# Kernel tuning notes

Measured on AMD Instinct MI355X. Metric: run time of the kernel, lower is better.

The kernel has to match this reference:

```python
import jax, jax.numpy as jnp
import numpy as np

N = 100_000      # nodes (single heterogeneous node type)
E = 1_600_000    # edges per relation (avg in-degree ~16)
D = 128          # in_feats
H = 128          # rep_dim
R = 3            # relations


def setup_inputs() -> dict:
    key = jax.random.key(0)
    ks = jax.random.split(key, 1 + 6 * R)
    inp = {"x": jax.random.normal(ks[0], (N, D), jnp.float32)}
    for r in range(R):
        k = ks[1 + 6 * r: 1 + 6 * (r + 1)]
        inp[f"src{r}"] = jax.random.randint(k[0], (E,), 0, N)
        inp[f"dst{r}"] = jax.random.randint(k[1], (E,), 0, N)
        inp[f"w{r}"] = jax.random.uniform(k[2], (E,), jnp.float32)
        inp[f"Wself{r}"] = jax.random.normal(k[3], (D, H), jnp.float32) * 0.05
        inp[f"Wneigh{r}"] = jax.random.normal(k[4], (D, H), jnp.float32) * 0.05
        inp[f"b{r}"] = jax.random.normal(k[5], (H,), jnp.float32) * 0.05
    return inp


def _sage_mean(x, src, dst, w, Wself, Wneigh, b):
    """DGL SAGEConv, aggregator='mean', edge_weight=w, activation=ReLU.

    h_N[v] = (sum_{e:(u->v)} w_e * x[u]) / max(in_deg(v), 1)
    out    = relu(x @ Wself + h_N @ Wneigh + b)
    """
    msg = x[src] * w[:, None]                                   # [E, D] gather
    s = jax.ops.segment_sum(msg, dst, num_segments=N)           # [N, D] scatter-add
    deg = jax.ops.segment_sum(jnp.ones_like(w), dst, num_segments=N)  # [N]
    h_neigh = s / jnp.maximum(deg, 1.0)[:, None]                # mean; 0 for isolated nodes
    return jax.nn.relu(x @ Wself + h_neigh @ Wneigh + b)


def reference(x,
              src0, dst0, w0,
              src1, dst1, w1,
              src2, dst2, w2,
              Wself0, Wneigh0, b0,
              Wself1, Wneigh1, b1,
              Wself2, Wneigh2, b2):
    # HeteroGraphConv(aggregate='mean'): average the per-relation SAGEConv outputs.
    o0 = _sage_mean(x, src0, dst0, w0, Wself0, Wneigh0, b0)
    o1 = _sage_mean(x, src1, dst1, w1, Wself1, Wneigh1, b1)
    o2 = _sage_mean(x, src2, dst2, w2, Wself2, Wneigh2, b2)
    return (o0 + o1 + o2) / 3.0
```

## Files before the change

### kernel.cpp

```cpp
#include <hip/hip_runtime.h>
#include <hip/hip_bf16.h>
#include <cstdio>
#include <cstdint>
#include <cstddef>

#define NN 100000
#define EE 1600000
#define DD 128

#define BKT 196
#define RSHIFT 9
#define RANGE 512
#define CAP 9500
#define EPB 2048
#define ABLK ((EE + EPB - 1) / EPB)

typedef __attribute__((ext_vector_type(8))) short short8;
typedef __attribute__((ext_vector_type(4))) float floatx4;

__device__ __forceinline__ float bf2f(unsigned short u) {
    union { unsigned int u; float f; } c;
    c.u = ((unsigned int)u) << 16;
    return c.f;
}
__device__ __forceinline__ unsigned short f2bf(float f) {
    union { float f; unsigned int u; } c;
    c.f = f;
    unsigned int lsb = (c.u >> 16) & 1u;
    c.u += 0x7fffu + lsb;
    return (unsigned short)(c.u >> 16);
}

__global__ void detect_kernel(const void* x, const void* w, const void* Wm,
                              const void* b, int* flags) {
    __shared__ int ok_s;
    int bid = blockIdx.x, tid = threadIdx.x;
    if (tid == 0) ok_s = 0;
    __syncthreads();
    const unsigned short* p;
    int n;
    if (bid == 0)      { p = (const unsigned short*)x;  n = 1024; }
    else if (bid == 1) { p = (const unsigned short*)w;  n = 1024; }
    else if (bid == 2) { p = (const unsigned short*)Wm; n = 1024; }
    else               { p = (const unsigned short*)b;  n = 128;  }
    int ok = 0;
    for (int i = tid; i < n; i += blockDim.x) {
        unsigned short u = p[i];
        int e = (u >> 7) & 0xff;
        if (u == 0 || u == 0x8000 || (e >= 90 && e <= 127)) ok++;
    }
    atomicAdd(&ok_s, ok);
    __syncthreads();
    if (tid == 0) flags[bid] = (ok_s * 4 >= n * 3) ? 1 : 0;
}

__global__ void conv_x_kernel(const void* src, unsigned short* dst, int n4,
                              const int* flag) {
    if (*flag) return;
    int i = blockIdx.x * blockDim.x + threadIdx.x;
    if (i >= n4) return;
    float4 f = ((const float4*)src)[i];
    uint2 o;
    o.x = (unsigned int)f2bf(f.x) | ((unsigned int)f2bf(f.y) << 16);
    o.y = (unsigned int)f2bf(f.z) | ((unsigned int)f2bf(f.w) << 16);
    ((uint2*)dst)[i] = o;
}

__global__ void conv_f32_kernel(const void* src, float* dst, int n,
                                const int* flag) {
    int i = blockIdx.x * blockDim.x + threadIdx.x;
    if (i >= n) return;
    if (*flag) dst[i] = bf2f(((const unsigned short*)src)[i]);
    else       dst[i] = ((const float*)src)[i];
}

__global__ void conv_transposeW_kernel(const void* W, unsigned short* wT,
                                       const int* flag) {
    int i = blockIdx.x * blockDim.x + threadIdx.x;
    int d = i >> 7, h = i & 127;
    unsigned short v;
    if (*flag) v = ((const unsigned short*)W)[i];
    else       v = f2bf(((const float*)W)[i]);
    wT[h * DD + d] = v;
}

__global__ void __launch_bounds__(256) binscatter_kernel(
    const int* __restrict__ srcp, const int* __restrict__ dstp,
    const void* __restrict__ wp, int* __restrict__ gcur,
    int2* __restrict__ ebin, const int* __restrict__ wflag) {
    __shared__ int hist[BKT];
    __shared__ int off[BKT];
    __shared__ int cur[BKT];
    __shared__ int gbase[BKT];
    __shared__ int scan[256];
    __shared__ int2 sorted[EPB];
    __shared__ unsigned char slotb[EPB];
    const int tid = threadIdx.x;
    const int base = blockIdx.x * EPB;
    for (int i = tid; i < BKT; i += 256) hist[i] = 0;
    __syncthreads();
    int myd[8];
#pragma unroll
    for (int k = 0; k < 8; k++) {
        int i = base + k * 256 + tid;
        int d = (i < EE) ? dstp[i] : -1;
        myd[k] = d;
        if (d >= 0) atomicAdd(&hist[d >> RSHIFT], 1);
    }
    __syncthreads();
    int hv = (tid < BKT) ? hist[tid] : 0;
    scan[tid] = hv;
    __syncthreads();
    for (int o = 1; o < 256; o <<= 1) {
        int v = (tid >= o) ? scan[tid - o] : 0;
        __syncthreads();
        scan[tid] += v;
        __syncthreads();
    }
    if (tid < BKT) { off[tid] = scan[tid] - hv; cur[tid] = scan[tid] - hv; }
    __syncthreads();
    const bool wbf = (*wflag != 0);
#pragma unroll
    for (int k = 0; k < 8; k++) {
        int d = myd[k];
        if (d < 0) continue;
        int i = base + k * 256 + tid;
        int b = d >> RSHIFT;
        int dloc = d - (b << RSHIFT);
        int s = srcp[i];
        float wv = wbf ? bf2f(((const unsigned short*)wp)[i])
                       : ((const float*)wp)[i];
        union { float f; int i; } c; c.f = wv;
        int pos = atomicAdd(&cur[b], 1);
        sorted[pos] = make_int2(s | (dloc << 17), c.i);
        slotb[pos] = (unsigned char)b;
    }
    __syncthreads();
    if (tid < BKT) {
        int cnt = hist[tid];
        gbase[tid] = cnt ? atomicAdd(&gcur[tid], cnt) : 0;
    }
    __syncthreads();
    const int total = min(EPB, EE - base);
    for (int i = tid; i < total; i += 256) {
        int b = slotb[i];
        int g = gbase[b] + (i - off[b]);
        if (g < CAP) ebin[(size_t)b * CAP + g] = sorted[i];
    }
}

__global__ void __launch_bounds__(256) bucketsort_kernel(
    const int2* __restrict__ ebin, const int* __restrict__ gcur,
    int2* __restrict__ es2, int2* __restrict__ ptrv) {
    __shared__ int hc[RANGE];
    __shared__ int off[RANGE];
    __shared__ int scan[256];
    const int b = blockIdx.x, tid = threadIdx.x;
    const int base = b * CAP;
    const int cnt = min(gcur[b], CAP);
    for (int i = tid; i < RANGE; i += 256) hc[i] = 0;
    __syncthreads();
    for (int i = tid; i < cnt; i += 256) {
        int dl = ebin[base + i].x >> 17;
        atomicAdd(&hc[dl], 1);
    }
    __syncthreads();
    int a0 = hc[2 * tid], a1 = hc[2 * tid + 1];
    scan[tid] = a0 + a1;
    __syncthreads();
    for (int o = 1; o < 256; o <<= 1) {
        int v = (tid >= o) ? scan[tid - o] : 0;
        __syncthreads();
        scan[tid] += v;
        __syncthreads();
    }
    int ex = scan[tid] - (a0 + a1);
    off[2 * tid] = ex;
    off[2 * tid + 1] = ex + a0;
    ptrv[b * RANGE + 2 * tid]     = make_int2(base + ex, a0);
    ptrv[b * RANGE + 2 * tid + 1] = make_int2(base + ex + a0, a1);
    __syncthreads();
    hc[2 * tid] = off[2 * tid];
    hc[2 * tid + 1] = off[2 * tid + 1];
    __syncthreads();
    for (int i = tid; i < cnt; i += 256) {
        int2 rec = ebin[base + i];
        int dl = rec.x >> 17;
        int p = atomicAdd(&hc[dl], 1);
        es2[base + p] = make_int2(rec.x & 0x1FFFF, rec.y);
    }
}

__global__ void __launch_bounds__(256) aggregate_kernel(
    const int2* __restrict__ es, const int2* __restrict__ ptrv,
    const unsigned short* __restrict__ xc, const void* __restrict__ xraw,
    const int* __restrict__ xflag, unsigned short* __restrict__ hout) {
    int wave = (blockIdx.x * blockDim.x + threadIdx.x) >> 6;
    int lane = threadIdx.x & 63;
    if (wave >= NN) return;
    const unsigned int* x32 = (*xflag) ? (const unsigned int*)xraw
                                       : (const unsigned int*)xc;
    int2 pc = ptrv[wave];
    int beg = pc.x, deg = pc.y, end = beg + deg;
    float a0 = 0.f, a1 = 0.f;
    int e = beg;
    for (; e + 4 <= end; e += 4) {
        int2 e0 = es[e], e1 = es[e + 1], e2 = es[e + 2], e3 = es[e + 3];
        unsigned int p0 = x32[(size_t)e0.x * 64 + lane];
        unsigned int p1 = x32[(size_t)e1.x * 64 + lane];
        unsigned int p2 = x32[(size_t)e2.x * 64 + lane];
        unsigned int p3 = x32[(size_t)e3.x * 64 + lane];
        union { int i; float f; } c0, c1, c2, c3;
        c0.i = e0.y; c1.i = e1.y; c2.i = e2.y; c3.i = e3.y;
        a0 += c0.f * bf2f((unsigned short)(p0 & 0xffff));
        a1 += c0.f * bf2f((unsigned short)(p0 >> 16));
        a0 += c1.f * bf2f((unsigned short)(p1 & 0xffff));
        a1 += c1.f * bf2f((unsigned short)(p1 >> 16));
        a0 += c2.f * bf2f((unsigned short)(p2 & 0xffff));
        a1 += c2.f * bf2f((unsigned short)(p2 >> 16));
        a0 += c3.f * bf2f((unsigned short)(p3 & 0xffff));
        a1 += c3.f * bf2f((unsigned short)(p3 >> 16));
    }
    for (; e < end; e++) {
        int2 e0 = es[e];
        unsigned int p0 = x32[(size_t)e0.x * 64 + lane];
        union { int i; float f; } c0; c0.i = e0.y;
        a0 += c0.f * bf2f((unsigned short)(p0 & 0xffff));
        a1 += c0.f * bf2f((unsigned short)(p0 >> 16));
    }
    float inv = 1.0f / (float)(deg > 1 ? deg : 1);
    unsigned int outv = ((unsigned int)f2bf(a1 * inv) << 16) | f2bf(a0 * inv);
    ((unsigned int*)hout)[(size_t)wave * 64 + lane] = outv;
}

__global__ void __launch_bounds__(256) output_kernel(
    const unsigned short* __restrict__ xc, const void* __restrict__ xraw,
    const unsigned short* __restrict__ h, const unsigned short* __restrict__ wT,
    const float* __restrict__ bc, void* out, const int* __restrict__ flag) {
    __shared__ unsigned short lds[DD * 136];
    const int tid = threadIdx.x;
    const int wv = tid >> 6, lane = tid & 63;
    const int tile = blockIdx.x * 4 + wv;
    const bool active = tile < (NN / 16);
    const int c = lane & 15, q = lane >> 4;
    const int nodeRow = tile * 16 + c;
    const int xbf = *flag;
    const unsigned short* xs = xbf ? (const unsigned short*)xraw : xc;

    short8 xfrag[4];
    if (active) {
#pragma unroll
        for (int kc = 0; kc < 4; kc++)
            xfrag[kc] = *(const short8*)(xs + (size_t)nodeRow * DD + kc * 32 +
                                         q * 8);
    }

    floatx4 outacc[8];
#pragma unroll
    for (int i = 0; i < 8; i++) outacc[i] = (floatx4){0.f, 0.f, 0.f, 0.f};

    for (int r = 0; r < 3; r++) {
        floatx4 acc[8];
#pragma unroll
        for (int i = 0; i < 8; i++) acc[i] = (floatx4){0.f, 0.f, 0.f, 0.f};
        for (int p = 0; p < 2; p++) {
            const unsigned short* Wg = wT + (size_t)(r * 2 + p) * DD * DD;
            __syncthreads();
            for (int chunk = tid; chunk < DD * DD / 8; chunk += 256) {
                int row = chunk >> 4, col8 = chunk & 15;
                short8 v = *(const short8*)(Wg + row * DD + col8 * 8);
                *(short8*)(&lds[row * 136 + col8 * 8]) = v;
            }
            __syncthreads();
            if (active) {
#pragma unroll
                for (int kc = 0; kc < 4; kc++) {
                    short8 afrag;
                    if (p == 0) {
                        afrag = xfrag[kc];
                    } else {
                        afrag = *(const short8*)(h + (size_t)r * NN * DD +
                                                 (size_t)nodeRow * DD +
                                                 kc * 32 + q * 8);
                    }
#pragma unroll
                    for (int nt = 0; nt < 8; nt++) {
                        short8 bfrag = *(const short8*)(
                            &lds[(nt * 16 + c) * 136 + kc * 32 + q * 8]);
                        acc[nt] = __builtin_amdgcn_mfma_f32_16x16x32_bf16(
                            afrag, bfrag, acc[nt], 0, 0, 0);
                    }
                }
            }
        }
        if (active) {
#pragma unroll
            for (int nt = 0; nt < 8; nt++) {
                float bv = bc[r * DD + nt * 16 + c];
#pragma unroll
                for (int i = 0; i < 4; i++) {
                    float v = acc[nt][i] + bv;
                    outacc[nt][i] += fmaxf(v, 0.f);
                }
            }
        }
    }
    if (active) {
        const float sc = 1.f / 3.f;
        if (xbf) {
            unsigned short* o = (unsigned short*)out;
#pragma unroll
            for (int nt = 0; nt < 8; nt++)
#pragma unroll
                for (int i = 0; i < 4; i++)
                    o[(size_t)(tile * 16 + q * 4 + i) * DD + nt * 16 + c] =
                        f2bf(outacc[nt][i] * sc);
        } else {
            float* o = (float*)out;
#pragma unroll
            for (int nt = 0; nt < 8; nt++)
#pragma unroll
                for (int i = 0; i < 4; i++)
                    o[(size_t)(tile * 16 + q * 4 + i) * DD + nt * 16 + c] =
                        outacc[nt][i] * sc;
        }
    }
}

extern "C" void kernel_launch(void* const* d_in, const int* in_sizes, int n_in,
                              void* d_out, int out_size, void* d_ws,
                              size_t ws_size, hipStream_t stream) {
    char* w = (char*)d_ws;
    size_t off = 0;
    auto alloc = [&](size_t bytes) {
        size_t o = off;
        off = (off + bytes + 255) & ~(size_t)255;
        return o;
    };
    size_t o_flags = alloc(4 * sizeof(int));
    size_t o_gcur  = alloc(BKT * sizeof(int));
    size_t o_bc    = alloc(3 * DD * sizeof(float));
    size_t o_wT    = alloc(6 * DD * DD * sizeof(unsigned short));
    size_t o_xc    = alloc((size_t)NN * DD * sizeof(unsigned short));
    size_t o_ebin  = alloc((size_t)BKT * CAP * sizeof(int2));
    size_t o_es2   = alloc((size_t)BKT * CAP * sizeof(int2));
    size_t o_ptrv  = alloc((size_t)BKT * RANGE * sizeof(int2));
    size_t o_h     = alloc((size_t)3 * NN * DD * sizeof(unsigned short));
    if (ws_size < off) {
        fprintf(stderr, "kernel_launch: ws_size=%zu < needed=%zu\n", ws_size,
                off);
        return;
    }
    int* flags          = (int*)(w + o_flags);
    int* gcur           = (int*)(w + o_gcur);
    float* bc           = (float*)(w + o_bc);
    unsigned short* wT  = (unsigned short*)(w + o_wT);
    unsigned short* xc  = (unsigned short*)(w + o_xc);
    int2* ebin          = (int2*)(w + o_ebin);
    int2* es2           = (int2*)(w + o_es2);
    int2* ptrv          = (int2*)(w + o_ptrv);
    unsigned short* hh  = (unsigned short*)(w + o_h);

    const void* x_in = d_in[0];

    detect_kernel<<<4, 256, 0, stream>>>(x_in, d_in[3], d_in[4], d_in[6],
                                         flags);
    conv_x_kernel<<<(NN * DD / 4 + 255) / 256, 256, 0, stream>>>(
        x_in, xc, NN * DD / 4, flags + 0);
    for (int r = 0; r < 3; r++) {
        int base = 1 + 6 * r;
        conv_transposeW_kernel<<<64, 256, 0, stream>>>(
            d_in[base + 3], wT + (size_t)(r * 2 + 0) * DD * DD, flags + 2);
        conv_transposeW_kernel<<<64, 256, 0, stream>>>(
            d_in[base + 4], wT + (size_t)(r * 2 + 1) * DD * DD, flags + 2);
        conv_f32_kernel<<<1, 128, 0, stream>>>(d_in[base + 5], bc + r * DD, DD,
                                               flags + 3);
    }

    for (int r = 0; r < 3; r++) {
        int base = 1 + 6 * r;
        const int* srcp = (const int*)d_in[base + 0];
        const int* dstp = (const int*)d_in[base + 1];
        hipMemsetAsync(gcur, 0, BKT * sizeof(int), stream);
        binscatter_kernel<<<ABLK, 256, 0, stream>>>(srcp, dstp, d_in[base + 2],
                                                    gcur, ebin, flags + 1);
        bucketsort_kernel<<<BKT, 256, 0, stream>>>(ebin, gcur, es2, ptrv);
        aggregate_kernel<<<(NN + 3) / 4, 256, 0, stream>>>(
            es2, ptrv, xc, x_in, flags + 0, hh + (size_t)r * NN * DD);
    }

    const int NTILES = NN / 16;
    output_kernel<<<(NTILES + 3) / 4, 256, 0, stream>>>(
        xc, x_in, hh, wT, bc, d_out, flags + 0);
}
```

Measured before the change: 616.7 us.

## Replace atomic bucket offsets with count-scan-place pass; unroll gather loop by 8

Splits the edge bucketing into three kernels: a per-block histogram, a per-bucket scan across blocks, and a placement pass that reads precomputed bases. This removes the global atomicAdd and the memset, and makes bucket order deterministic, but reads dst twice and adds two kernel launches per relation. The aggregation loop is unrolled from 4 to 8 edges to keep more gathers in flight, and the bf16 unpack is done with simpler bit ops.

```diff
diff --git a/kernel.cpp b/kernel.cpp
--- a/kernel.cpp
+++ b/kernel.cpp
@@ -21,6 +21,16 @@
 __device__ __forceinline__ float bf2f(unsigned short u) {
     union { unsigned int u; float f; } c;
     c.u = ((unsigned int)u) << 16;
+    return c.f;
+}
+__device__ __forceinline__ float hi2f(unsigned int p) {
+    union { unsigned int u; float f; } c;
+    c.u = p & 0xffff0000u;
+    return c.f;
+}
+__device__ __forceinline__ float lo2f(unsigned int p) {
+    union { unsigned int u; float f; } c;
+    c.u = p << 16;
     return c.f;
 }
 __device__ __forceinline__ unsigned short f2bf(float f) {
@@ -84,9 +94,58 @@
     wT[h * DD + d] = v;
 }
 
-__global__ void __launch_bounds__(256) binscatter_kernel(
+__global__ void __launch_bounds__(256) countA_kernel(
+    const int* __restrict__ dstp, int* __restrict__ cnts) {
+    __shared__ int hist[BKT];
+    const int tid = threadIdx.x;
+    const int base = blockIdx.x * EPB;
+    for (int i = tid; i < BKT; i += 256) hist[i] = 0;
+    __syncthreads();
+#pragma unroll
+    for (int k = 0; k < 8; k++) {
+        int i = base + k * 256 + tid;
+        if (i < EE) atomicAdd(&hist[dstp[i] >> RSHIFT], 1);
+    }
+    __syncthreads();
+    for (int i = tid; i < BKT; i += 256)
+        cnts[(size_t)blockIdx.x * BKT + i] = hist[i];
+}
+
+__global__ void __launch_bounds__(256) scanA_kernel(
+    const int* __restrict__ cnts, int* __restrict__ bases,
+    int* __restrict__ gcur) {
+    __shared__ int s[256];
+    const int b = blockIdx.x, tid = threadIdx.x;
+    const int per = (ABLK + 255) / 256;
+    int v[4];
+    int sum = 0;
+#pragma unroll
+    for (int k = 0; k < 4; k++) {
+        int idx = tid * per + k;
+        v[k] = (idx < ABLK) ? cnts[(size_t)idx * BKT + b] : 0;
+        sum += v[k];
+    }
+    s[tid] = sum;
+    __syncthreads();
+    for (int o = 1; o < 256; o <<= 1) {
+        int t = (tid >= o) ? s[tid - o] : 0;
+        __syncthreads();
+        s[tid] += t;
+        __syncthreads();
+    }
+    int running = s[tid] - sum;
+#pragma unroll
+    for (int k = 0; k < 4; k++) {
+        int idx = tid * per + k;
+        if (idx < ABLK) bases[(size_t)idx * BKT + b] = running;
+        running += v[k];
+    }
+    if (tid == 255) gcur[b] = s[255];
+}
+
+__global__ void __launch_bounds__(256) placeA_kernel(
     const int* __restrict__ srcp, const int* __restrict__ dstp,
-    const void* __restrict__ wp, int* __restrict__ gcur,
+    const void* __restrict__ wp, const int* __restrict__ bases,
     int2* __restrict__ ebin, const int* __restrict__ wflag) {
     __shared__ int hist[BKT];
     __shared__ int off[BKT];
@@ -117,7 +176,11 @@
         scan[tid] += v;
         __syncthreads();
     }
-    if (tid < BKT) { off[tid] = scan[tid] - hv; cur[tid] = scan[tid] - hv; }
+    if (tid < BKT) {
+        off[tid] = scan[tid] - hv;
+        cur[tid] = scan[tid] - hv;
+        gbase[tid] = bases[(size_t)blockIdx.x * BKT + tid];
+    }
     __syncthreads();
     const bool wbf = (*wflag != 0);
 #pragma unroll
@@ -136,11 +199,6 @@
         slotb[pos] = (unsigned char)b;
     }
     __syncthreads();
-    if (tid < BKT) {
-        int cnt = hist[tid];
-        gbase[tid] = cnt ? atomicAdd(&gcur[tid], cnt) : 0;
-    }
-    __syncthreads();
     const int total = min(EPB, EE - base);
     for (int i = tid; i < total; i += 256) {
         int b = slotb[i];
@@ -204,29 +262,43 @@
     int beg = pc.x, deg = pc.y, end = beg + deg;
     float a0 = 0.f, a1 = 0.f;
     int e = beg;
-    for (; e + 4 <= end; e += 4) {
-        int2 e0 = es[e], e1 = es[e + 1], e2 = es[e + 2], e3 = es[e + 3];
-        unsigned int p0 = x32[(size_t)e0.x * 64 + lane];
-        unsigned int p1 = x32[(size_t)e1.x * 64 + lane];
-        unsigned int p2 = x32[(size_t)e2.x * 64 + lane];
-        unsigned int p3 = x32[(size_t)e3.x * 64 + lane];
-        union { int i; float f; } c0, c1, c2, c3;
-        c0.i = e0.y; c1.i = e1.y; c2.i = e2.y; c3.i = e3.y;
-        a0 += c0.f * bf2f((unsigned short)(p0 & 0xffff));
-        a1 += c0.f * bf2f((unsigned short)(p0 >> 16));
-        a0 += c1.f * bf2f((unsigned short)(p1 & 0xffff));
-        a1 += c1.f * bf2f((unsigned short)(p1 >> 16));
-        a0 += c2.f * bf2f((unsigned short)(p2 & 0xffff));
-        a1 += c2.f * bf2f((unsigned short)(p2 >> 16));
-        a0 += c3.f * bf2f((unsigned short)(p3 & 0xffff));
-        a1 += c3.f * bf2f((unsigned short)(p3 >> 16));
-    }
-    for (; e < end; e++) {
-        int2 e0 = es[e];
-        unsigned int p0 = x32[(size_t)e0.x * 64 + lane];
-        union { int i; float f; } c0; c0.i = e0.y;
-        a0 += c0.f * bf2f((unsigned short)(p0 & 0xffff));
-        a1 += c0.f * bf2f((unsigned short)(p0 >> 16));
+    for (; e + 8 <= end; e += 8) {
+        int2 r0 = es[e],     r1 = es[e + 1], r2 = es[e + 2], r3 = es[e + 3];
+        int2 r4 = es[e + 4], r5 = es[e + 5], r6 = es[e + 6], r7 = es[e + 7];
+        unsigned int p0 = x32[(size_t)r0.x * 64 + lane];
+        unsigned int p1 = x32[(size_t)r1.x * 64 + lane];
+        unsigned int p2 = x32[(size_t)r2.x * 64 + lane];
+        unsigned int p3 = x32[(size_t)r3.x * 64 + lane];
+        unsigned int p4 = x32[(size_t)r4.x * 64 + lane];
+        unsigned int p5 = x32[(size_t)r5.x * 64 + lane];
+        unsigned int p6 = x32[(size_t)r6.x * 64 + lane];
+        unsigned int p7 = x32[(size_t)r7.x * 64 + lane];
+        union { int i; float f; } c0, c1, c2, c3, c4, c5, c6, c7;
+        c0.i = r0.y; c1.i = r1.y; c2.i = r2.y; c3.i = r3.y;
+        c4.i = r4.y; c5.i = r5.y; c6.i = r6.y; c7.i = r7.y;
+        a0 += c0.f * lo2f(p0); a1 += c0.f * hi2f(p0);
+        a0 += c1.f * lo2f(p1); a1 += c1.f * hi2f(p1);
+        a0 += c2.f * lo2f(p2); a1 += c2.f * hi2f(p2);
+        a0 += c3.f * lo2f(p3); a1 += c3.f * hi2f(p3);
+        a0 += c4.f * lo2f(p4); a1 += c4.f * hi2f(p4);
+        a0 += c5.f * lo2f(p5); a1 += c5.f * hi2f(p5);
+        a0 += c6.f * lo2f(p6); a1 += c6.f * hi2f(p6);
+        a0 += c7.f * lo2f(p7); a1 += c7.f * hi2f(p7);
+    }
+    for (; e + 2 <= end; e += 2) {
+        int2 r0 = es[e], r1 = es[e + 1];
+        unsigned int p0 = x32[(size_t)r0.x * 64 + lane];
+        unsigned int p1 = x32[(size_t)r1.x * 64 + lane];
+        union { int i; float f; } c0, c1;
+        c0.i = r0.y; c1.i = r1.y;
+        a0 += c0.f * lo2f(p0); a1 += c0.f * hi2f(p0);
+        a0 += c1.f * lo2f(p1); a1 += c1.f * hi2f(p1);
+    }
+    if (e < end) {
+        int2 r0 = es[e];
+        unsigned int p0 = x32[(size_t)r0.x * 64 + lane];
+        union { int i; float f; } c0; c0.i = r0.y;
+        a0 += c0.f * lo2f(p0); a1 += c0.f * hi2f(p0);
     }
     float inv = 1.0f / (float)(deg > 1 ? deg : 1);
     unsigned int outv = ((unsigned int)f2bf(a1 * inv) << 16) | f2bf(a0 * inv);
@@ -342,6 +414,8 @@
     size_t o_bc    = alloc(3 * DD * sizeof(float));
     size_t o_wT    = alloc(6 * DD * DD * sizeof(unsigned short));
     size_t o_xc    = alloc((size_t)NN * DD * sizeof(unsigned short));
+    size_t o_cnts  = alloc((size_t)ABLK * BKT * sizeof(int));
+    size_t o_bases = alloc((size_t)ABLK * BKT * sizeof(int));
     size_t o_ebin  = alloc((size_t)BKT * CAP * sizeof(int2));
     size_t o_es2   = alloc((size_t)BKT * CAP * sizeof(int2));
     size_t o_ptrv  = alloc((size_t)BKT * RANGE * sizeof(int2));
@@ -356,6 +430,8 @@
     float* bc           = (float*)(w + o_bc);
     unsigned short* wT  = (unsigned short*)(w + o_wT);
     unsigned short* xc  = (unsigned short*)(w + o_xc);
+    int* cnts           = (int*)(w + o_cnts);
+    int* bases          = (int*)(w + o_bases);
     int2* ebin          = (int2*)(w + o_ebin);
     int2* es2           = (int2*)(w + o_es2);
     int2* ptrv          = (int2*)(w + o_ptrv);
@@ -381,9 +457,10 @@
         int base = 1 + 6 * r;
         const int* srcp = (const int*)d_in[base + 0];
         const int* dstp = (const int*)d_in[base + 1];
-        hipMemsetAsync(gcur, 0, BKT * sizeof(int), stream);
-        binscatter_kernel<<<ABLK, 256, 0, stream>>>(srcp, dstp, d_in[base + 2],
-                                                    gcur, ebin, flags + 1);
+        countA_kernel<<<ABLK, 256, 0, stream>>>(dstp, cnts);
+        scanA_kernel<<<BKT, 256, 0, stream>>>(cnts, bases, gcur);
+        placeA_kernel<<<ABLK, 256, 0, stream>>>(srcp, dstp, d_in[base + 2],
+                                                bases, ebin, flags + 1);
         bucketsort_kernel<<<BKT, 256, 0, stream>>>(ebin, gcur, es2, ptrv);
         aggregate_kernel<<<(NN + 3) / 4, 256, 0, stream>>>(
             es2, ptrv, xc, x_in, flags + 0, hh + (size_t)r * NN * DD);
```

Result: faster. 578.2 us (-6.3%).
